# Performance work log

Measured on AMD Instinct MI355X. Metric: run time of the kernel, lower is better.

## Reference

```python
import jax, jax.numpy as jnp
import numpy as np

N = 1048576
NUM_FREQS = 4
NUM_DIM = 3
NUM_QUANTS = 80
NUM_FEATS = 4
MIN_LOG2_FREQ = 1.0
MAX_LOG2_FREQ = 6.0
NUM_LINES = 2 * NUM_FREQS * NUM_DIM  # sin/cos x freq x axis = 24
LATENT = NUM_LINES * NUM_FEATS       # 96


def setup_inputs() -> dict:
    key = jax.random.key(0)
    ks = jax.random.split(key, 8)
    positions = jax.random.uniform(ks[0], (N, NUM_DIM), jnp.float32, -1.0, 1.0)
    d = jax.random.normal(ks[1], (N, NUM_DIM), jnp.float32)
    directions = d / jnp.linalg.norm(d, axis=-1, keepdims=True)
    grid = jax.random.normal(ks[2], (NUM_LINES, NUM_QUANTS, NUM_FEATS), jnp.float32) * 0.1
    w_geom1 = jax.random.normal(ks[3], (LATENT, 64), jnp.float32) * (1.0 / np.sqrt(LATENT))
    w_geom2 = jax.random.normal(ks[4], (64, 16), jnp.float32) * (1.0 / 8.0)
    w_color1 = jax.random.normal(ks[5], (31, 64), jnp.float32) * (1.0 / np.sqrt(31.0))
    w_color2 = jax.random.normal(ks[6], (64, 64), jnp.float32) * (1.0 / 8.0)
    w_color3 = jax.random.normal(ks[7], (64, 3), jnp.float32) * (1.0 / 8.0)
    return {"positions": positions, "directions": directions, "grid": grid,
            "w_geom1": w_geom1, "w_geom2": w_geom2,
            "w_color1": w_color1, "w_color2": w_color2, "w_color3": w_color3}


@jax.custom_vjp
def trunc_exp(x):
    return jnp.exp(x)

def _te_fwd(x):
    return jnp.exp(x), x

def _te_bwd(x, g):
    return (g * jnp.exp(jnp.clip(x, -15.0, 15.0)),)

trunc_exp.defvjp(_te_fwd, _te_bwd)


def spherical_harmonics16(d):
    # degree-4 (l=0..3) real SH basis, 16 components, torch-ngp coefficients
    x, y, z = d[:, 0], d[:, 1], d[:, 2]
    xx, yy, zz = x * x, y * y, z * z
    xy, yz, xz = x * y, y * z, x * z
    return jnp.stack([
        jnp.full_like(x, 0.28209479177387814),
        -0.48860251190291987 * y,
        0.48860251190291987 * z,
        -0.48860251190291987 * x,
        1.0925484305920792 * xy,
        -1.0925484305920792 * yz,
        0.94617469575755997 * zz - 0.31539156525251999,
        -1.0925484305920792 * xz,
        0.54627421529603959 * (xx - yy),
        -0.59004358992664352 * y * (3.0 * xx - yy),
        2.8906114426405538 * xy * z,
        -0.45704579946446572 * y * (4.0 * zz - xx - yy),
        0.37317633259011546 * z * (2.0 * zz - 3.0 * xx - 3.0 * yy),
        -0.45704579946446572 * x * (4.0 * zz - xx - yy),
        1.4453057213202769 * z * (xx - yy),
        -0.59004358992664352 * x * (xx - 3.0 * yy),
    ], axis=-1)  # [N, 16]


def qff1_encode(positions, grid):
    # frequencies 2^linspace(min,max,F)
    freqs = 2.0 ** jnp.linspace(MIN_LOG2_FREQ, MAX_LOG2_FREQ, NUM_FREQS).astype(jnp.float32)
    # phase: [N, D, F]
    p = positions[:, :, None] * freqs[None, None, :]
    coords = jnp.concatenate([jnp.sin(p), jnp.cos(p)], axis=-1)  # [N, D, 2F]
    coords = coords.transpose(0, 2, 1).reshape(positions.shape[0], NUM_LINES)  # [N, L]
    # map [-1,1] -> continuous grid coord and linearly interpolate 1D lines
    u = (coords + 1.0) * 0.5 * (NUM_QUANTS - 1)
    i0 = jnp.clip(jnp.floor(u).astype(jnp.int32), 0, NUM_QUANTS - 2)
    w = (u - i0.astype(u.dtype))[..., None]  # [N, L, 1]
    lidx = jnp.arange(NUM_LINES)[None, :]
    g0 = grid[lidx, i0]      # [N, L, C]
    g1 = grid[lidx, i0 + 1]  # [N, L, C]
    feat = g0 * (1.0 - w) + g1 * w
    return feat.reshape(positions.shape[0], LATENT)


def _forward(positions, directions, grid, w_geom1, w_geom2, w_color1, w_color2, w_color3):
    enc = qff1_encode(positions, grid)                    # [N, 96]
    h = jax.nn.relu(enc @ w_geom1)                        # [N, 64]
    f = h @ w_geom2                                       # [N, 16]
    raw_sigma, feature = f[:, :1], f[:, 1:]
    density = trunc_exp(raw_sigma - 1.0)                  # [N, 1]
    sh = spherical_harmonics16(directions)                # [N, 16]
    hc = jnp.concatenate([sh, feature], axis=-1)          # [N, 31]
    hc = jax.nn.relu(hc @ w_color1)
    hc = jax.nn.relu(hc @ w_color2)
    rgb = jax.nn.sigmoid(hc @ w_color3)                   # [N, 3]
    return rgb, density


def reference(positions, directions, grid, w_geom1, w_geom2, w_color1, w_color2, w_color3):
    return _forward(positions, directions, grid, w_geom1, w_geom2, w_color1, w_color2, w_color3)
```

## Files before the change

### kernel.cpp

```cpp
#include <hip/hip_runtime.h>
#include <stdint.h>


typedef _Float16 half8  __attribute__((ext_vector_type(8)));
typedef _Float16 h2     __attribute__((ext_vector_type(2)));
typedef float    f32x16 __attribute__((ext_vector_type(16)));

union FragU { uint32_t u[4]; uint4 q; half8 h; };
union H2U   { uint32_t u; h2 h; };

static __device__ __forceinline__ h2 bch2(uint32_t v) { H2U x; x.u = v; return x.h; }
static __device__ __forceinline__ uint32_t bcu(h2 v)  { H2U x; x.h = v; return x.u; }

static __device__ __forceinline__ h2 cvtpk(float lo, float hi) {
  return __builtin_bit_cast(h2, __builtin_amdgcn_cvt_pkrtz(lo, hi));
}
static __device__ __forceinline__ uint32_t pkrtz(float lo, float hi) {
  return bcu(cvtpk(lo, hi));
}
static __device__ __forceinline__ void plswap_u(uint32_t &a, uint32_t &b) {
  asm("v_permlane32_swap_b32 %0, %1" : "+v"(a), "+v"(b));
}
static __device__ __forceinline__ void plswap_f(float &a, float &b) {
  asm("v_permlane32_swap_b32 %0, %1" : "+v"(a), "+v"(b));
}
static __device__ __forceinline__ half8 mk_frag(uint32_t a, uint32_t b, uint32_t c, uint32_t d) {
  FragU f; f.u[0] = a; f.u[1] = b; f.u[2] = c; f.u[3] = d; return f.h;
}
static __device__ __forceinline__ uint32_t maxz(uint32_t v) {
  h2 h = bch2(v); h = __builtin_elementwise_max(h, (h2)(_Float16)0.0f); return bcu(h);
}
static __device__ __forceinline__ unsigned short f16b(float v) {
  _Float16 h = (_Float16)v; return __builtin_bit_cast(unsigned short, h);
}

#define MFMA(A, B, C) __builtin_amdgcn_mfma_f32_32x32x16_f16((A), (B), (C), 0, 0, 0)

#define W1OFF   0
#define W2OFF   13312
#define WC1OFF  17920
#define WC2OFF  23040
#define WC3OFF  32256
#define GROFF   36864
#define LDSZ    52224
#define WBYTES  36864

static __device__ __forceinline__ half8 ldw(const unsigned char* s, int row, int off) {
  FragU f; f.q = *(const uint4*)(s + row + off); return f.h;
}

template<int BASE, bool RELU>
static __device__ __forceinline__ half8 packB(const f32x16& a) {
  uint32_t x = pkrtz(a[BASE + 0], a[BASE + 1]);
  uint32_t z = pkrtz(a[BASE + 2], a[BASE + 3]);
  uint32_t y = pkrtz(a[BASE + 4], a[BASE + 5]);
  uint32_t w = pkrtz(a[BASE + 6], a[BASE + 7]);
  if (RELU) { x = maxz(x); z = maxz(z); y = maxz(y); w = maxz(w); }
  plswap_u(x, y);
  plswap_u(z, w);
  return mk_frag(x, z, y, w);
}

struct Pre {
  float m[6];
  int   gb[6];
  int   a13, a9, a5;
};

template<int J>
static __device__ __forceinline__ void gather(const Pre& pre, float q0, float q1, float q2,
                                              const unsigned char* lds,
                                              uint32_t& w01, uint32_t& w23) {
  constexpr int jm = J % 6;
  constexpr int DIMP[6] = {0, 1, 1, 2, 2, 0};
  float q = (DIMP[jm] == 0) ? q0 : ((DIMP[jm] == 1) ? q1 : q2);
  float r = fmaf(q, pre.m[jm], (J < 6) ? 0.0f : 0.25f);
  r = __builtin_amdgcn_fractf(r);
  float s = __builtin_amdgcn_sinf(r);
  float u  = fmaf(s, 39.5f, 39.5f);
  float fu = floorf(u);
  fu = fminf(fu, 78.0f);
  float w = u - fu;
  int addr = (pre.gb[jm] + (int)fu + ((J < 6) ? 0 : 960)) << 3;
  const uint2* pe = (const uint2*)(lds + addr);
  uint2 ua = pe[0];
  uint2 ub = pe[1];
  h2 a0 = bch2(ua.x), a1 = bch2(ua.y), b0 = bch2(ub.x), b1 = bch2(ub.y);
  h2 wh = cvtpk(w, w);
  h2 f01 = __builtin_elementwise_fma(b0 - a0, wh, a0);
  h2 f23 = __builtin_elementwise_fma(b1 - a1, wh, a1);
  w01 = bcu(f01);
  w23 = bcu(f23);
}

template<int T>
static __device__ __forceinline__ half8 enc2(const Pre& pre, float q0, float q1, float q2,
                                             const unsigned char* lds) {
  uint32_t a, b, c, d;
  gather<2 * T + 0>(pre, q0, q1, q2, lds, a, b);
  gather<2 * T + 1>(pre, q0, q1, q2, lds, c, d);
  return mk_frag(a, b, c, d);
}

__global__ __launch_bounds__(256, 3)
void qff_fwd(const float* __restrict__ pos, const float* __restrict__ dir,
             const float* __restrict__ grid,
             const float* __restrict__ w1, const float* __restrict__ w2,
             const float* __restrict__ wc1, const float* __restrict__ wc2,
             const float* __restrict__ wc3,
             float* __restrict__ out, int Npts) {
  __shared__ __align__(16) unsigned char smem[LDSZ];
  const int tid = threadIdx.x;

  for (int i = tid; i < WBYTES / 4; i += 256) ((uint32_t*)smem)[i] = 0;
  __syncthreads();
  for (int i = tid; i < 6144; i += 256)
    *(unsigned short*)(smem + W1OFF  + (i & 63) * 208 + (i >> 6) * 2) = f16b(w1[i]);
  for (int i = tid; i < 1024; i += 256)
    *(unsigned short*)(smem + W2OFF  + (i & 15) * 144 + (i >> 4) * 2) = f16b(w2[i]);
  for (int i = tid; i < 1984; i += 256)
    *(unsigned short*)(smem + WC1OFF + (i & 63) * 80  + (i >> 6) * 2) = f16b(wc1[i]);
  for (int i = tid; i < 4096; i += 256)
    *(unsigned short*)(smem + WC2OFF + (i & 63) * 144 + (i >> 6) * 2) = f16b(wc2[i]);
  for (int i = tid; i < 192; i += 256)
    *(unsigned short*)(smem + WC3OFF + (i % 3) * 144 + (i / 3) * 2) = f16b(wc3[i]);
  for (int i = tid; i < 3840; i += 256) {
    float2 v = ((const float2*)grid)[i];
    *(uint32_t*)(smem + GROFF + i * 4) = (((uint32_t)f16b(v.y)) << 16) | f16b(v.x);
  }
  __syncthreads();

  const int lane = tid & 63;
  const int wid  = tid >> 6;
  const int g    = lane >> 5;
  const int o    = lane & 31;

  constexpr float IV = 0.15915494309189535f;
  constexpr float F0 = 2.0f, F1 = 6.349604207872798f, F2 = 20.158736798317971f, F3 = 64.0f;
  const float M0c[6] = {F0*IV, F0*IV, F1*IV, F1*IV, F2*IV, F3*IV};
  const float M1c[6] = {F0*IV, F1*IV, F2*IV, F2*IV, F3*IV, F3*IV};
  const int   GB0[6] = {4608, 4688, 4928, 5008, 5248, 5328};
  const int   GB1[6] = {4768, 4848, 5088, 5168, 5408, 5488};
  Pre pre;
#pragma unroll
  for (int j = 0; j < 6; ++j) {
    pre.m[j]  = g ? M1c[j] : M0c[j];
    pre.gb[j] = g ? GB1[j] : GB0[j];
  }
  pre.a13 = o * 208 + g * 16;
  pre.a9  = o * 144 + g * 16;
  pre.a5  = o * 80  + g * 16;

  const f32x16 Z = {0,0,0,0, 0,0,0,0, 0,0,0,0, 0,0,0,0};
  const int ntile = Npts >> 7;
  int tb = blockIdx.x;
  if (tb >= ntile) return;

  int p = (tb << 7) + (wid << 5) + o;
  float px = pos[3*p+0], py = pos[3*p+1], pz = pos[3*p+2];
  float dx = dir[3*p+0], dy = dir[3*p+1], dz = dir[3*p+2];

  for (; tb < ntile; tb += gridDim.x) {
    int tbn = tb + gridDim.x;
    int pn  = ((tbn < ntile ? tbn : ntile - 1) << 7) + (wid << 5) + o;
    float npx = pos[3*pn+0], npy = pos[3*pn+1], npz = pos[3*pn+2];
    float ndx = dir[3*pn+0], ndy = dir[3*pn+1], ndz = dir[3*pn+2];

    float q0 = g ? pz : px;
    float q1 = g ? px : py;
    float q2 = g ? py : pz;

    f32x16 acc0 = Z, acc1 = Z;
#define L1STEP(T) { half8 bf = enc2<T>(pre, q0, q1, q2, smem); \
                    acc0 = MFMA(ldw(smem, pre.a13, W1OFF + T*32), bf, acc0); \
                    acc1 = MFMA(ldw(smem, pre.a13, W1OFF + 6656 + T*32), bf, acc1); }
    L1STEP(0) L1STEP(1) L1STEP(2) L1STEP(3) L1STEP(4) L1STEP(5)
#undef L1STEP

    half8 hb0 = packB<0, true>(acc0), hb1 = packB<8, true>(acc0);
    half8 hb2 = packB<0, true>(acc1), hb3 = packB<8, true>(acc1);

    f32x16 acc2 = Z;
    acc2 = MFMA(ldw(smem, pre.a9, W2OFF +  0), hb0, acc2);
    acc2 = MFMA(ldw(smem, pre.a9, W2OFF + 32), hb1, acc2);
    acc2 = MFMA(ldw(smem, pre.a9, W2OFF + 64), hb2, acc2);
    acc2 = MFMA(ldw(smem, pre.a9, W2OFF + 96), hb3, acc2);
    float sigma = __expf(acc2[0] - 1.0f);

    float xx = dx*dx, yy = dy*dy, zz = dz*dz;
    float xy = dx*dy, yz = dy*dz, xz = dx*dz;
    float s0, s1, s2, s3, s4, s5, s6, s7;
    if (g == 0) {
      s0 = 0.28209479177387814f;
      s1 = -0.48860251190291987f * dy;
      s2 =  0.48860251190291987f * dz;
      s3 = -0.48860251190291987f * dx;
      s4 =  1.0925484305920792f * xy;
      s5 = -1.0925484305920792f * yz;
      s6 =  0.94617469575756f * zz - 0.31539156525252f;
      s7 = -1.0925484305920792f * xz;
    } else {
      s0 =  0.5462742152960396f * (xx - yy);
      s1 = -0.5900435899266435f * dy * (3.0f * xx - yy);
      s2 =  2.890611442640554f * xy * dz;
      s3 = -0.4570457994644657f * dy * (4.0f * zz - xx - yy);
      s4 =  0.37317633259011546f * dz * (2.0f * zz - 3.0f * xx - 3.0f * yy);
      s5 = -0.4570457994644657f * dx * (4.0f * zz - xx - yy);
      s6 =  1.445305721320277f * dz * (xx - yy);
      s7 = -0.5900435899266435f * dx * (xx - 3.0f * yy);
    }
    half8 shB = mk_frag(pkrtz(s0, s1), pkrtz(s2, s3), pkrtz(s4, s5), pkrtz(s6, s7));

    uint32_t e0 = pkrtz(acc2[1], acc2[2]);
    uint32_t e2 = pkrtz(acc2[5], acc2[6]);
    plswap_u(e0, e2);
    float a3 = acc2[3], b7 = acc2[7];
    plswap_f(a3, b7);
    float cc0 = acc2[0], d4 = acc2[4];
    plswap_f(cc0, d4);
    uint32_t e1 = pkrtz(a3, d4);
    uint32_t e3 = pkrtz(b7, acc2[4]);
    half8 featB = mk_frag(e0, e1, e2, e3);

    f32x16 acc3a = Z, acc3b = Z;
    acc3a = MFMA(ldw(smem, pre.a5, WC1OFF +  0), shB,   acc3a);
    acc3a = MFMA(ldw(smem, pre.a5, WC1OFF + 32), featB, acc3a);
    acc3b = MFMA(ldw(smem, pre.a5, WC1OFF + 2560 +  0), shB,   acc3b);
    acc3b = MFMA(ldw(smem, pre.a5, WC1OFF + 2560 + 32), featB, acc3b);

    half8 g2b0 = packB<0, true>(acc3a), g2b1 = packB<8, true>(acc3a);
    half8 g2b2 = packB<0, true>(acc3b), g2b3 = packB<8, true>(acc3b);

    f32x16 acc4a = Z, acc4b = Z;
    acc4a = MFMA(ldw(smem, pre.a9, WC2OFF +  0), g2b0, acc4a);
    acc4a = MFMA(ldw(smem, pre.a9, WC2OFF + 32), g2b1, acc4a);
    acc4a = MFMA(ldw(smem, pre.a9, WC2OFF + 64), g2b2, acc4a);
    acc4a = MFMA(ldw(smem, pre.a9, WC2OFF + 96), g2b3, acc4a);
    acc4b = MFMA(ldw(smem, pre.a9, WC2OFF + 4608 +  0), g2b0, acc4b);
    acc4b = MFMA(ldw(smem, pre.a9, WC2OFF + 4608 + 32), g2b1, acc4b);
    acc4b = MFMA(ldw(smem, pre.a9, WC2OFF + 4608 + 64), g2b2, acc4b);
    acc4b = MFMA(ldw(smem, pre.a9, WC2OFF + 4608 + 96), g2b3, acc4b);

    half8 g3b0 = packB<0, true>(acc4a), g3b1 = packB<8, true>(acc4a);
    half8 g3b2 = packB<0, true>(acc4b), g3b3 = packB<8, true>(acc4b);

    f32x16 acc5 = Z;
    acc5 = MFMA(ldw(smem, pre.a9, WC3OFF +  0), g3b0, acc5);
    acc5 = MFMA(ldw(smem, pre.a9, WC3OFF + 32), g3b1, acc5);
    acc5 = MFMA(ldw(smem, pre.a9, WC3OFF + 64), g3b2, acc5);
    acc5 = MFMA(ldw(smem, pre.a9, WC3OFF + 96), g3b3, acc5);

    if (lane < 32) {
      float rr = __builtin_amdgcn_rcpf(1.0f + __expf(-acc5[0]));
      float gg = __builtin_amdgcn_rcpf(1.0f + __expf(-acc5[1]));
      float bb = __builtin_amdgcn_rcpf(1.0f + __expf(-acc5[2]));
      out[3 * p + 0] = rr;
      out[3 * p + 1] = gg;
      out[3 * p + 2] = bb;
      out[3 * Npts + p] = sigma;
    }

    p = pn;
    px = npx; py = npy; pz = npz;
    dx = ndx; dy = ndy; dz = ndz;
  }
}

extern "C" void kernel_launch(void* const* d_in, const int* in_sizes, int n_in,
                              void* d_out, int out_size, void* d_ws, size_t ws_size,
                              hipStream_t stream) {
  const float* pos  = (const float*)d_in[0];
  const float* dirs = (const float*)d_in[1];
  const float* grid = (const float*)d_in[2];
  const float* w1   = (const float*)d_in[3];
  const float* w2   = (const float*)d_in[4];
  const float* wc1  = (const float*)d_in[5];
  const float* wc2  = (const float*)d_in[6];
  const float* wc3  = (const float*)d_in[7];
  float* out = (float*)d_out;
  const int Npts = in_sizes[0] / 3;

  qff_fwd<<<dim3(768), dim3(256), 0, stream>>>(pos, dirs, grid, w1, w2, wc1, wc2, wc3,
                                               out, Npts);
}
```

Baseline: 53.14 us.

## Split grid features into planar LDS layout and double block size

Grid features in LDS are split into two planes per line (features 0-1 and 2-3, each 320 bytes apart), so each gather does four 32-bit reads instead of two 64-bit reads, which may change bank conflict behaviour. Floor is replaced by truncation with an integer clamp. Blocks grow from 256 to 512 threads with 8 waves per block and 256 points per tile, which amortises the per-block weight staging over more waves. The risk is extra LDS instructions per gather and higher per-block register and LDS pressure under the new launch bounds.

```diff
diff --git a/kernel.cpp b/kernel.cpp
--- a/kernel.cpp
+++ b/kernel.cpp
@@ -63,7 +63,7 @@
 
 struct Pre {
   float m[6];
-  int   gb[6];
+  int   gbs[12];
   int   a13, a9, a5;
 };
 
@@ -77,18 +77,18 @@
   float r = fmaf(q, pre.m[jm], (J < 6) ? 0.0f : 0.25f);
   r = __builtin_amdgcn_fractf(r);
   float s = __builtin_amdgcn_sinf(r);
-  float u  = fmaf(s, 39.5f, 39.5f);
-  float fu = floorf(u);
-  fu = fminf(fu, 78.0f);
-  float w = u - fu;
-  int addr = (pre.gb[jm] + (int)fu + ((J < 6) ? 0 : 960)) << 3;
-  const uint2* pe = (const uint2*)(lds + addr);
-  uint2 ua = pe[0];
-  uint2 ub = pe[1];
-  h2 a0 = bch2(ua.x), a1 = bch2(ua.y), b0 = bch2(ub.x), b1 = bch2(ub.y);
+  float u = fmaf(s, 39.5f, 39.5f);
+  int i0 = (int)u;
+  i0 = i0 < 0 ? 0 : (i0 > 78 ? 78 : i0);
+  float w = u - (float)i0;
+  const unsigned char* base = lds + pre.gbs[J] + (i0 << 2);
+  uint32_t a0 = *(const uint32_t*)(base);
+  uint32_t b0 = *(const uint32_t*)(base + 4);
+  uint32_t a1 = *(const uint32_t*)(base + 320);
+  uint32_t b1 = *(const uint32_t*)(base + 324);
   h2 wh = cvtpk(w, w);
-  h2 f01 = __builtin_elementwise_fma(b0 - a0, wh, a0);
-  h2 f23 = __builtin_elementwise_fma(b1 - a1, wh, a1);
+  h2 f01 = __builtin_elementwise_fma(bch2(b0) - bch2(a0), wh, bch2(a0));
+  h2 f23 = __builtin_elementwise_fma(bch2(b1) - bch2(a1), wh, bch2(a1));
   w01 = bcu(f01);
   w23 = bcu(f23);
 }
@@ -102,7 +102,7 @@
   return mk_frag(a, b, c, d);
 }
 
-__global__ __launch_bounds__(256, 3)
+__global__ __launch_bounds__(512, 6)
 void qff_fwd(const float* __restrict__ pos, const float* __restrict__ dir,
              const float* __restrict__ grid,
              const float* __restrict__ w1, const float* __restrict__ w2,
@@ -112,21 +112,24 @@
   __shared__ __align__(16) unsigned char smem[LDSZ];
   const int tid = threadIdx.x;
 
-  for (int i = tid; i < WBYTES / 4; i += 256) ((uint32_t*)smem)[i] = 0;
+  for (int i = tid; i < WBYTES / 4; i += 512) ((uint32_t*)smem)[i] = 0;
   __syncthreads();
-  for (int i = tid; i < 6144; i += 256)
+  for (int i = tid; i < 6144; i += 512)
     *(unsigned short*)(smem + W1OFF  + (i & 63) * 208 + (i >> 6) * 2) = f16b(w1[i]);
-  for (int i = tid; i < 1024; i += 256)
+  for (int i = tid; i < 1024; i += 512)
     *(unsigned short*)(smem + W2OFF  + (i & 15) * 144 + (i >> 4) * 2) = f16b(w2[i]);
-  for (int i = tid; i < 1984; i += 256)
+  for (int i = tid; i < 1984; i += 512)
     *(unsigned short*)(smem + WC1OFF + (i & 63) * 80  + (i >> 6) * 2) = f16b(wc1[i]);
-  for (int i = tid; i < 4096; i += 256)
+  for (int i = tid; i < 4096; i += 512)
     *(unsigned short*)(smem + WC2OFF + (i & 63) * 144 + (i >> 6) * 2) = f16b(wc2[i]);
-  for (int i = tid; i < 192; i += 256)
+  for (int i = tid; i < 192; i += 512)
     *(unsigned short*)(smem + WC3OFF + (i % 3) * 144 + (i / 3) * 2) = f16b(wc3[i]);
-  for (int i = tid; i < 3840; i += 256) {
-    float2 v = ((const float2*)grid)[i];
-    *(uint32_t*)(smem + GROFF + i * 4) = (((uint32_t)f16b(v.y)) << 16) | f16b(v.x);
+  for (int i = tid; i < 1920; i += 512) {
+    float4 v = ((const float4*)grid)[i];
+    int line = i / 80, q = i - line * 80;
+    uint32_t* dst = (uint32_t*)(smem + GROFF + line * 640 + q * 4);
+    dst[0]  = (((uint32_t)f16b(v.y)) << 16) | f16b(v.x);
+    dst[80] = (((uint32_t)f16b(v.w)) << 16) | f16b(v.z);
   }
   __syncthreads();
 
@@ -139,30 +142,32 @@
   constexpr float F0 = 2.0f, F1 = 6.349604207872798f, F2 = 20.158736798317971f, F3 = 64.0f;
   const float M0c[6] = {F0*IV, F0*IV, F1*IV, F1*IV, F2*IV, F3*IV};
   const float M1c[6] = {F0*IV, F1*IV, F2*IV, F2*IV, F3*IV, F3*IV};
-  const int   GB0[6] = {4608, 4688, 4928, 5008, 5248, 5328};
-  const int   GB1[6] = {4768, 4848, 5088, 5168, 5408, 5488};
+  const int   LNS0[6] = {0, 1, 4, 5, 8, 9};
+  const int   LNS1[6] = {2, 3, 6, 7, 10, 11};
   Pre pre;
 #pragma unroll
   for (int j = 0; j < 6; ++j) {
-    pre.m[j]  = g ? M1c[j] : M0c[j];
-    pre.gb[j] = g ? GB1[j] : GB0[j];
+    pre.m[j] = g ? M1c[j] : M0c[j];
+    int ln = g ? LNS1[j] : LNS0[j];
+    pre.gbs[j]     = GROFF + ln * 640;
+    pre.gbs[j + 6] = GROFF + (ln + 12) * 640;
   }
   pre.a13 = o * 208 + g * 16;
   pre.a9  = o * 144 + g * 16;
   pre.a5  = o * 80  + g * 16;
 
   const f32x16 Z = {0,0,0,0, 0,0,0,0, 0,0,0,0, 0,0,0,0};
-  const int ntile = Npts >> 7;
+  const int ntile = Npts >> 8;
   int tb = blockIdx.x;
   if (tb >= ntile) return;
 
-  int p = (tb << 7) + (wid << 5) + o;
+  int p = (tb << 8) + (wid << 5) + o;
   float px = pos[3*p+0], py = pos[3*p+1], pz = pos[3*p+2];
   float dx = dir[3*p+0], dy = dir[3*p+1], dz = dir[3*p+2];
 
   for (; tb < ntile; tb += gridDim.x) {
     int tbn = tb + gridDim.x;
-    int pn  = ((tbn < ntile ? tbn : ntile - 1) << 7) + (wid << 5) + o;
+    int pn  = ((tbn < ntile ? tbn : ntile - 1) << 8) + (wid << 5) + o;
     float npx = pos[3*pn+0], npy = pos[3*pn+1], npz = pos[3*pn+2];
     float ndx = dir[3*pn+0], ndy = dir[3*pn+1], ndz = dir[3*pn+2];
 
@@ -280,6 +285,6 @@
   float* out = (float*)d_out;
   const int Npts = in_sizes[0] / 3;
 
-  qff_fwd<<<dim3(768), dim3(256), 0, stream>>>(pos, dirs, grid, w1, w2, wc1, wc2, wc3,
+  qff_fwd<<<dim3(768), dim3(512), 0, stream>>>(pos, dirs, grid, w1, w2, wc1, wc2, wc3,
                                                out, Npts);
 }
```

Result: slower. 84.99 us (+59.9%).
